# Optimization experiments

Hardware: AMD Instinct MI355X
Metric: run time of the kernel (lower is better)

The kernel has to match this reference:

```python
import jax, jax.numpy as jnp
import numpy as np

WS = 11      # window_size
SIGMA = 1.5
C1 = 0.01 ** 2
C2 = 0.03 ** 2


def _window(channel):
    g = np.exp(-((np.arange(WS) - WS // 2) ** 2) / (2.0 * SIGMA ** 2))
    g = (g / g.sum()).astype(np.float32)
    w2 = np.outer(g, g)  # [WS, WS]
    return jnp.asarray(np.broadcast_to(w2, (channel, 1, WS, WS)).copy())


def _blur(x, w, channel):
    pad = WS // 2
    return jax.lax.conv_general_dilated(
        x, w, window_strides=(1, 1), padding=[(pad, pad), (pad, pad)],
        dimension_numbers=("NCHW", "OIHW", "NCHW"),
        feature_group_count=channel)


def _ssim(img1, img2, w, channel):
    mu1 = _blur(img1, w, channel)
    mu2 = _blur(img2, w, channel)
    mu1_sq = mu1 * mu1
    mu2_sq = mu2 * mu2
    mu1_mu2 = mu1 * mu2
    sigma1_sq = _blur(img1 * img1, w, channel) - mu1_sq
    sigma2_sq = _blur(img2 * img2, w, channel) - mu2_sq
    sigma12 = _blur(img1 * img2, w, channel) - mu1_mu2
    ssim_map = ((2.0 * mu1_mu2 + C1) * (2.0 * sigma12 + C2)) / (
        (mu1_sq + mu2_sq + C1) * (sigma1_sq + sigma2_sq + C2))
    return ssim_map.mean()  # size_average=True


def setup_inputs() -> dict:
    key = jax.random.key(0)
    k1, k2, k3 = jax.random.split(key, 3)
    B, C, H, W = 16, 3, 512, 512
    return {
        "fused_img": jax.random.uniform(k1, (B, C, H, W), dtype=jnp.float32),
        "source_img1": jax.random.uniform(k2, (B, C, H, W), dtype=jnp.float32),
        "source_img2": jax.random.uniform(k3, (B, C, H, W), dtype=jnp.float32),
    }


def reference(fused_img, source_img1, source_img2):
    channel = fused_img.shape[1]
    w = _window(channel).astype(fused_img.dtype)
    ssim1 = _ssim(fused_img, source_img1, w, channel)
    ssim2 = _ssim(fused_img, source_img2, w, channel)
    return 1.0 - (ssim1 + ssim2) / 2.0
```

## Files before the change

### kernel.cpp

```cpp
#include <hip/hip_runtime.h>
#include <cmath>

#define HALO 5
#define TSX 32
#define TILE_H 64
#define NCHUNK 4
#define CH 16
#define RING 26
#define HSTR 36
#define PLANE (RING * HSTR)
#define WIDTH 512
#define HEIGHT 512

struct GW { float g[11]; };

__device__ __forceinline__ float ssim2(float mu1, float mu2,
                                       float x2b, float y2b, float xyb)
{
    const float C1 = 1e-4f, C2 = 9e-4f;
    float mu12 = mu1 * mu2;
    float num  = (2.f * mu12 + C1) * (2.f * (xyb - mu12) + C2);
    float den  = (mu1 * mu1 + mu2 * mu2 + C1) *
                 ((x2b - mu1 * mu1) + (y2b - mu2 * mu2) + C2);
    return num * __builtin_amdgcn_rcpf(den);
}

template<bool CHK>
__device__ __forceinline__ float tile_compute(
    const float* __restrict__ fI, const float* __restrict__ aI,
    const float* __restrict__ bI, float (* __restrict__ hb)[PLANE],
    const GW& gw, int tid, int x0, int y0, size_t pbase)
{
    const int rA  = tid >> 3;
    const int qA  = tid & 7;
    const int gx0 = x0 + 4 * qA - 8;
    const int jB  = tid & 31;
    const int rgB = tid >> 5;
    const bool actB = (rgB < 4);

    float part = 0.f;

    #pragma unroll 1
    for (int c = 0; c < NCHUNK; ++c) {
        if (c) __syncthreads();

        const int nA = c ? CH : RING;
        if (rA < nA) {
            const int t = c ? (16 * c + 10 + rA) : rA;
            int slot = t;
            slot -= (slot >= RING) ? RING : 0;
            slot -= (slot >= RING) ? RING : 0;
            const int yy = y0 - HALO + t;
            const bool yok = CHK ? ((unsigned)yy < (unsigned)HEIGHT) : true;
            const float* rowf = fI + pbase + (size_t)yy * WIDTH;
            const float* rowa = aI + pbase + (size_t)yy * WIDTH;
            const float* rowb = bI + pbase + (size_t)yy * WIDTH;

            float acc[4][8];
            #pragma unroll
            for (int jj = 0; jj < 4; ++jj)
                #pragma unroll
                for (int q = 0; q < 8; ++q) acc[jj][q] = 0.f;

            #pragma unroll
            for (int k = 0; k < 5; ++k) {
                const int g = gx0 + 4 * k;
                float4 vf, va, vb;
                if (CHK) {
                    const bool ok = yok && ((unsigned)g <= (unsigned)(WIDTH - 4));
                    vf = ok ? *(const float4*)(rowf + g) : make_float4(0,0,0,0);
                    va = ok ? *(const float4*)(rowa + g) : make_float4(0,0,0,0);
                    vb = ok ? *(const float4*)(rowb + g) : make_float4(0,0,0,0);
                } else {
                    vf = *(const float4*)(rowf + g);
                    va = *(const float4*)(rowa + g);
                    vb = *(const float4*)(rowb + g);
                }
                const float fs[4] = { vf.x, vf.y, vf.z, vf.w };
                const float as[4] = { va.x, va.y, va.z, va.w };
                const float bs[4] = { vb.x, vb.y, vb.z, vb.w };
                #pragma unroll
                for (int cc = 0; cc < 4; ++cc) {
                    const int tt = 4 * k + cc - 3;
                    if (tt < 0 || tt > 13) continue;
                    const float f = fs[cc], a = as[cc], b = bs[cc];
                    float p[8];
                    p[0] = f; p[1] = a; p[2] = b;
                    p[3] = f * f; p[4] = a * a; p[5] = b * b;
                    p[6] = f * a; p[7] = f * b;
                    #pragma unroll
                    for (int jj = 0; jj < 4; ++jj) {
                        const int u = tt - jj;
                        if (u >= 0 && u <= 10) {
                            const float w = gw.g[u];
                            #pragma unroll
                            for (int q = 0; q < 8; ++q)
                                acc[jj][q] = fmaf(w, p[q], acc[jj][q]);
                        }
                    }
                }
            }
            #pragma unroll
            for (int q = 0; q < 8; ++q)
                *(float4*)(&hb[q][slot * HSTR + 4 * qA]) =
                    make_float4(acc[0][q], acc[1][q], acc[2][q], acc[3][q]);
        }
        __syncthreads();

        if (actB) {
            int sb = 16 * c + 4 * rgB;
            sb -= (sb >= RING) ? RING : 0;
            sb -= (sb >= RING) ? RING : 0;
            float acc2[4][8];
            #pragma unroll
            for (int ri = 0; ri < 4; ++ri)
                #pragma unroll
                for (int q = 0; q < 8; ++q) acc2[ri][q] = 0.f;
            #pragma unroll
            for (int k = 0; k < 14; ++k) {
                int s = sb + k;
                s -= (s >= RING) ? RING : 0;
                const float* hp = &hb[0][s * HSTR + jB];
                float hv[8];
                #pragma unroll
                for (int q = 0; q < 8; ++q) hv[q] = hp[q * PLANE];
                #pragma unroll
                for (int ri = 0; ri < 4; ++ri) {
                    const int u = k - ri;
                    if (u >= 0 && u <= 10) {
                        const float w = gw.g[u];
                        #pragma unroll
                        for (int q = 0; q < 8; ++q)
                            acc2[ri][q] = fmaf(w, hv[q], acc2[ri][q]);
                    }
                }
            }
            #pragma unroll
            for (int ri = 0; ri < 4; ++ri) {
                part += ssim2(acc2[ri][0], acc2[ri][1],
                              acc2[ri][3], acc2[ri][4], acc2[ri][6]);
                part += ssim2(acc2[ri][0], acc2[ri][2],
                              acc2[ri][3], acc2[ri][5], acc2[ri][7]);
            }
        }
    }
    return part;
}

__global__ __launch_bounds__(256, 4)
void ssim_tile(const float* __restrict__ fI, const float* __restrict__ aI,
               const float* __restrict__ bI, float* __restrict__ bsum,
               GW gw)
{
    __shared__ __align__(16) float hb[8][PLANE];
    __shared__ float red[4];

    const int tid = threadIdx.x;
    const int x0 = blockIdx.x * TSX;
    const int y0 = blockIdx.y * TILE_H;
    const size_t pbase = (size_t)blockIdx.z * (size_t)(WIDTH * HEIGHT);

    const bool interior = (blockIdx.x > 0) && (blockIdx.x < gridDim.x - 1) &&
                          (blockIdx.y > 0) && (blockIdx.y < gridDim.y - 1);

    float part = interior
        ? tile_compute<false>(fI, aI, bI, hb, gw, tid, x0, y0, pbase)
        : tile_compute<true >(fI, aI, bI, hb, gw, tid, x0, y0, pbase);

    #pragma unroll
    for (int off = 32; off > 0; off >>= 1) part += __shfl_down(part, off);
    if ((tid & 63) == 0) red[tid >> 6] = part;
    __syncthreads();
    if (tid == 0) {
        int bid = blockIdx.x + gridDim.x * (blockIdx.y + gridDim.y * blockIdx.z);
        bsum[bid] = red[0] + red[1] + red[2] + red[3];
    }
}

__global__ __launch_bounds__(256)
void ssim_final(const float* __restrict__ bsum, float* __restrict__ out,
                int nb, float invTwoN)
{
    __shared__ float sred[4];
    float s = 0.f;
    for (int i = threadIdx.x; i < nb; i += 256) s += bsum[i];
    #pragma unroll
    for (int off = 32; off > 0; off >>= 1) s += __shfl_down(s, off);
    if ((threadIdx.x & 63) == 0) sred[threadIdx.x >> 6] = s;
    __syncthreads();
    if (threadIdx.x == 0)
        out[0] = 1.f - (sred[0] + sred[1] + sred[2] + sred[3]) * invTwoN;
}

extern "C" void kernel_launch(void* const* d_in, const int* in_sizes, int n_in,
                              void* d_out, int out_size, void* d_ws, size_t ws_size,
                              hipStream_t stream)
{
    const float* f  = (const float*)d_in[0];
    const float* s1 = (const float*)d_in[1];
    const float* s2 = (const float*)d_in[2];
    float* out  = (float*)d_out;
    float* bsum = (float*)d_ws;

    const int N = in_sizes[0];
    const int planes = N / (WIDTH * HEIGHT);

    GW gw;
    double gd[11], gs = 0.0;
    for (int i = 0; i < 11; ++i) {
        double d = (double)(i - 5);
        gd[i] = exp(-(d * d) / 4.5);
        gs += gd[i];
    }
    for (int i = 0; i < 11; ++i) gw.g[i] = (float)(gd[i] / gs);

    dim3 grid(WIDTH / TSX, HEIGHT / TILE_H, planes);
    const int nb = (WIDTH / TSX) * (HEIGHT / TILE_H) * planes;
    ssim_tile<<<grid, dim3(256), 0, stream>>>(f, s1, s2, bsum, gw);
    ssim_final<<<1, dim3(256), 0, stream>>>(bsum, out, nb, 0.5f / (float)N);
}
```

Before: 246.9 us.

## Double tile height so all threads run vertical pass, split boundary checks by axis

Raises the tile height from 64 to 128 rows with 32-row chunks and a 42-row ring buffer. This cuts the halo recompute overhead per output row, and all 8 thread groups now do the vertical pass instead of only 4. The horizontal pass loops when there are more than 32 rows, and the boundary checks are split into separate x and y template flags so edge tiles only pay for the checks they need. The cost is more shared memory (42×36×8 floats) and a lower occupancy hint (3 blocks/SM), and the grid has half as many blocks.

```diff
diff --git a/kernel.cpp b/kernel.cpp
--- a/kernel.cpp
+++ b/kernel.cpp
@@ -3,10 +3,10 @@
 
 #define HALO 5
 #define TSX 32
-#define TILE_H 64
+#define TILE_H 128
 #define NCHUNK 4
-#define CH 16
-#define RING 26
+#define CH 32
+#define RING 42
 #define HSTR 36
 #define PLANE (RING * HSTR)
 #define WIDTH 512
@@ -25,7 +25,7 @@
     return num * __builtin_amdgcn_rcpf(den);
 }
 
-template<bool CHK>
+template<bool CX, bool CY>
 __device__ __forceinline__ float tile_compute(
     const float* __restrict__ fI, const float* __restrict__ aI,
     const float* __restrict__ bI, float (* __restrict__ hb)[PLANE],
@@ -36,7 +36,6 @@
     const int gx0 = x0 + 4 * qA - 8;
     const int jB  = tid & 31;
     const int rgB = tid >> 5;
-    const bool actB = (rgB < 4);
 
     float part = 0.f;
 
@@ -45,13 +44,15 @@
         if (c) __syncthreads();
 
         const int nA = c ? CH : RING;
-        if (rA < nA) {
-            const int t = c ? (16 * c + 10 + rA) : rA;
+        #pragma unroll 1
+        for (int t0 = rA; t0 < nA; t0 += 32) {
+            const int t = c ? (CH * c + 2 * HALO + t0) : t0;
             int slot = t;
             slot -= (slot >= RING) ? RING : 0;
             slot -= (slot >= RING) ? RING : 0;
+            slot -= (slot >= RING) ? RING : 0;
             const int yy = y0 - HALO + t;
-            const bool yok = CHK ? ((unsigned)yy < (unsigned)HEIGHT) : true;
+            const bool yok = CY ? ((unsigned)yy < (unsigned)HEIGHT) : true;
             const float* rowf = fI + pbase + (size_t)yy * WIDTH;
             const float* rowa = aI + pbase + (size_t)yy * WIDTH;
             const float* rowb = bI + pbase + (size_t)yy * WIDTH;
@@ -62,40 +63,42 @@
                 #pragma unroll
                 for (int q = 0; q < 8; ++q) acc[jj][q] = 0.f;
 
-            #pragma unroll
-            for (int k = 0; k < 5; ++k) {
-                const int g = gx0 + 4 * k;
-                float4 vf, va, vb;
-                if (CHK) {
-                    const bool ok = yok && ((unsigned)g <= (unsigned)(WIDTH - 4));
-                    vf = ok ? *(const float4*)(rowf + g) : make_float4(0,0,0,0);
-                    va = ok ? *(const float4*)(rowa + g) : make_float4(0,0,0,0);
-                    vb = ok ? *(const float4*)(rowb + g) : make_float4(0,0,0,0);
-                } else {
-                    vf = *(const float4*)(rowf + g);
-                    va = *(const float4*)(rowa + g);
-                    vb = *(const float4*)(rowb + g);
-                }
-                const float fs[4] = { vf.x, vf.y, vf.z, vf.w };
-                const float as[4] = { va.x, va.y, va.z, va.w };
-                const float bs[4] = { vb.x, vb.y, vb.z, vb.w };
+            if (yok) {
                 #pragma unroll
-                for (int cc = 0; cc < 4; ++cc) {
-                    const int tt = 4 * k + cc - 3;
-                    if (tt < 0 || tt > 13) continue;
-                    const float f = fs[cc], a = as[cc], b = bs[cc];
-                    float p[8];
-                    p[0] = f; p[1] = a; p[2] = b;
-                    p[3] = f * f; p[4] = a * a; p[5] = b * b;
-                    p[6] = f * a; p[7] = f * b;
+                for (int k = 0; k < 5; ++k) {
+                    const int g = gx0 + 4 * k;
+                    float4 vf, va, vb;
+                    if (CX) {
+                        const bool ok = ((unsigned)g <= (unsigned)(WIDTH - 4));
+                        vf = ok ? *(const float4*)(rowf + g) : make_float4(0,0,0,0);
+                        va = ok ? *(const float4*)(rowa + g) : make_float4(0,0,0,0);
+                        vb = ok ? *(const float4*)(rowb + g) : make_float4(0,0,0,0);
+                    } else {
+                        vf = *(const float4*)(rowf + g);
+                        va = *(const float4*)(rowa + g);
+                        vb = *(const float4*)(rowb + g);
+                    }
+                    const float fs[4] = { vf.x, vf.y, vf.z, vf.w };
+                    const float as[4] = { va.x, va.y, va.z, va.w };
+                    const float bs[4] = { vb.x, vb.y, vb.z, vb.w };
                     #pragma unroll
-                    for (int jj = 0; jj < 4; ++jj) {
-                        const int u = tt - jj;
-                        if (u >= 0 && u <= 10) {
-                            const float w = gw.g[u];
-                            #pragma unroll
-                            for (int q = 0; q < 8; ++q)
-                                acc[jj][q] = fmaf(w, p[q], acc[jj][q]);
+                    for (int cc = 0; cc < 4; ++cc) {
+                        const int tt = 4 * k + cc - 3;
+                        if (tt < 0 || tt > 13) continue;
+                        const float f = fs[cc], a = as[cc], b = bs[cc];
+                        float p[8];
+                        p[0] = f; p[1] = a; p[2] = b;
+                        p[3] = f * f; p[4] = a * a; p[5] = b * b;
+                        p[6] = f * a; p[7] = f * b;
+                        #pragma unroll
+                        for (int jj = 0; jj < 4; ++jj) {
+                            const int u = tt - jj;
+                            if (u >= 0 && u <= 10) {
+                                const float w = gw.g[u];
+                                #pragma unroll
+                                for (int q = 0; q < 8; ++q)
+                                    acc[jj][q] = fmaf(w, p[q], acc[jj][q]);
+                            }
                         }
                     }
                 }
@@ -107,47 +110,45 @@
         }
         __syncthreads();
 
-        if (actB) {
-            int sb = 16 * c + 4 * rgB;
-            sb -= (sb >= RING) ? RING : 0;
-            sb -= (sb >= RING) ? RING : 0;
-            float acc2[4][8];
-            #pragma unroll
-            for (int ri = 0; ri < 4; ++ri)
-                #pragma unroll
-                for (int q = 0; q < 8; ++q) acc2[ri][q] = 0.f;
-            #pragma unroll
-            for (int k = 0; k < 14; ++k) {
-                int s = sb + k;
-                s -= (s >= RING) ? RING : 0;
-                const float* hp = &hb[0][s * HSTR + jB];
-                float hv[8];
-                #pragma unroll
-                for (int q = 0; q < 8; ++q) hv[q] = hp[q * PLANE];
-                #pragma unroll
-                for (int ri = 0; ri < 4; ++ri) {
-                    const int u = k - ri;
-                    if (u >= 0 && u <= 10) {
-                        const float w = gw.g[u];
-                        #pragma unroll
-                        for (int q = 0; q < 8; ++q)
-                            acc2[ri][q] = fmaf(w, hv[q], acc2[ri][q]);
-                    }
+        int sb = CH * c + 4 * rgB;
+        sb -= (sb >= RING) ? RING : 0;
+        sb -= (sb >= RING) ? RING : 0;
+        float acc2[4][8];
+        #pragma unroll
+        for (int ri = 0; ri < 4; ++ri)
+            #pragma unroll
+            for (int q = 0; q < 8; ++q) acc2[ri][q] = 0.f;
+        #pragma unroll
+        for (int k = 0; k < 14; ++k) {
+            int s = sb + k;
+            s -= (s >= RING) ? RING : 0;
+            const float* hp = &hb[0][s * HSTR + jB];
+            float hv[8];
+            #pragma unroll
+            for (int q = 0; q < 8; ++q) hv[q] = hp[q * PLANE];
+            #pragma unroll
+            for (int ri = 0; ri < 4; ++ri) {
+                const int u = k - ri;
+                if (u >= 0 && u <= 10) {
+                    const float w = gw.g[u];
+                    #pragma unroll
+                    for (int q = 0; q < 8; ++q)
+                        acc2[ri][q] = fmaf(w, hv[q], acc2[ri][q]);
                 }
             }
-            #pragma unroll
-            for (int ri = 0; ri < 4; ++ri) {
-                part += ssim2(acc2[ri][0], acc2[ri][1],
-                              acc2[ri][3], acc2[ri][4], acc2[ri][6]);
-                part += ssim2(acc2[ri][0], acc2[ri][2],
-                              acc2[ri][3], acc2[ri][5], acc2[ri][7]);
-            }
+        }
+        #pragma unroll
+        for (int ri = 0; ri < 4; ++ri) {
+            part += ssim2(acc2[ri][0], acc2[ri][1],
+                          acc2[ri][3], acc2[ri][4], acc2[ri][6]);
+            part += ssim2(acc2[ri][0], acc2[ri][2],
+                          acc2[ri][3], acc2[ri][5], acc2[ri][7]);
         }
     }
     return part;
 }
 
-__global__ __launch_bounds__(256, 4)
+__global__ __launch_bounds__(256, 3)
 void ssim_tile(const float* __restrict__ fI, const float* __restrict__ aI,
                const float* __restrict__ bI, float* __restrict__ bsum,
                GW gw)
@@ -160,12 +161,18 @@
     const int y0 = blockIdx.y * TILE_H;
     const size_t pbase = (size_t)blockIdx.z * (size_t)(WIDTH * HEIGHT);
 
-    const bool interior = (blockIdx.x > 0) && (blockIdx.x < gridDim.x - 1) &&
-                          (blockIdx.y > 0) && (blockIdx.y < gridDim.y - 1);
-
-    float part = interior
-        ? tile_compute<false>(fI, aI, bI, hb, gw, tid, x0, y0, pbase)
-        : tile_compute<true >(fI, aI, bI, hb, gw, tid, x0, y0, pbase);
+    const bool ex = (blockIdx.x == 0) || (blockIdx.x == gridDim.x - 1);
+    const bool ey = (blockIdx.y == 0) || (blockIdx.y == gridDim.y - 1);
+
+    float part;
+    if (!ex && !ey)
+        part = tile_compute<false, false>(fI, aI, bI, hb, gw, tid, x0, y0, pbase);
+    else if (!ex)
+        part = tile_compute<false, true >(fI, aI, bI, hb, gw, tid, x0, y0, pbase);
+    else if (!ey)
+        part = tile_compute<true,  false>(fI, aI, bI, hb, gw, tid, x0, y0, pbase);
+    else
+        part = tile_compute<true,  true >(fI, aI, bI, hb, gw, tid, x0, y0, pbase);
 
     #pragma unroll
     for (int off = 32; off > 0; off >>= 1) part += __shfl_down(part, off);
```

After: 265.6 us. 1.08x slower.
